# Performance work log

Hardware: AMD Instinct MI355X
Metric: run time of the kernel (lower is better)

The kernel has to match this reference:

```python
import jax, jax.numpy as jnp
import numpy as np
import math

E = 512
H = 2048
P = 128  # attention_limit

def _make_params(key):
    ks = jax.random.split(key, 6)
    s = 0.02
    p = {}
    p['wq'] = jax.random.normal(ks[0], (E, E), jnp.float32) * s
    p['bq'] = jnp.zeros((E,), jnp.float32)
    p['wk'] = jax.random.normal(ks[1], (E, E), jnp.float32) * s
    p['bk'] = jnp.zeros((E,), jnp.float32)
    p['wv'] = jax.random.normal(ks[2], (E, E), jnp.float32) * s
    p['bv'] = jnp.zeros((E,), jnp.float32)
    p['w1'] = jax.random.normal(ks[3], (E, H), jnp.float32) * s
    p['b1'] = jnp.zeros((H,), jnp.float32)
    p['w2'] = jax.random.normal(ks[4], (H, E), jnp.float32) * s
    p['b2'] = jnp.zeros((E,), jnp.float32)
    p['ln1_w'] = jnp.ones((E,), jnp.float32)
    p['ln1_b'] = jnp.zeros((E,), jnp.float32)
    p['ln2_w'] = jnp.ones((E,), jnp.float32)
    p['ln2_b'] = jnp.zeros((E,), jnp.float32)
    return p

def setup_inputs() -> dict:
    key = jax.random.key(0)
    kx, kp = jax.random.split(key)
    inp = {'x': jax.random.normal(kx, (2, 1024, E), jnp.float32)}
    inp.update(_make_params(kp))
    return inp

def _layernorm(x, w, b, eps=1e-5):
    mu = jnp.mean(x, axis=-1, keepdims=True)
    var = jnp.mean((x - mu) ** 2, axis=-1, keepdims=True)
    return (x - mu) / jnp.sqrt(var + eps) * w + b

def _forward(x, wq, bq, wk, bk, wv, bv, w1, b1, w2, b2, ln1_w, ln1_b, ln2_w, ln2_b):
    B, S, Ed = x.shape
    # "RoPE" is actually additive sinusoidal PE in the source
    pos = jnp.arange(S, dtype=jnp.float32)[:, None]
    div = jnp.exp(jnp.arange(0, Ed, 2, dtype=jnp.float32) * (-math.log(10000.0) / Ed))
    pe = jnp.zeros((S, Ed), jnp.float32)
    pe = pe.at[:, 0::2].set(jnp.sin(pos * div))
    pe = pe.at[:, 1::2].set(jnp.cos(pos * div))
    x = x + pe[None]

    # local attention: pad x first, then apply K/V linears (padded rows -> bias)
    x_ext = jnp.pad(x, ((0, 0), (P, P), (0, 0)))
    q = x @ wq + bq                      # [B,S,E]
    k_ext = x_ext @ wk + bk              # [B,S+2P,E]
    v_ext = x_ext @ wv + bv
    W = 2 * P + 1
    win_idx = jnp.arange(S)[:, None] + jnp.arange(W)[None, :]  # [S,W]
    k_win = k_ext[:, win_idx]            # [B,S,W,E]
    v_win = v_ext[:, win_idx]            # [B,S,W,E]
    energy = jnp.einsum('bse,bswe->bsw', q, k_win) / jnp.sqrt(jnp.float32(Ed))
    attn = jax.nn.softmax(energy, axis=-1)
    attn_out = jnp.einsum('bsw,bswe->bse', attn, v_win)

    x = _layernorm(attn_out + x, ln1_w, ln1_b)
    ff = jnp.maximum(x @ w1 + b1, 0.0) @ w2 + b2
    return _layernorm(ff + x, ln2_w, ln2_b)

def reference(x, wq, bq, wk, bk, wv, bv, w1, b1, w2, b2, ln1_w, ln1_b, ln2_w, ln2_b):
    return _forward(x, wq, bq, wk, bk, wv, bv, w1, b1, w2, b2, ln1_w, ln1_b, ln2_w, ln2_b)
```

## Files before the change

### kernel.cpp

```cpp
#include <hip/hip_runtime.h>
#include <hip/hip_bf16.h>

#define S_LEN 1024
#define E_DIM 512
#define H_DIM 2048
#define P_PAD 128
#define EXTA 1296
#define BS_ROWS 2048

typedef __attribute__((ext_vector_type(8))) short bf16x8;
typedef __attribute__((ext_vector_type(4))) float f32x4;

__device__ inline ushort f2bf(float x) {
  union { float f; unsigned u; } c; c.f = x;
  unsigned u = c.u;
  u += 0x7fffu + ((u >> 16) & 1u);
  return (ushort)(u >> 16);
}

__device__ inline void gload16(ushort* dst, const ushort* src) {
  __builtin_amdgcn_global_load_lds(
      (const __attribute__((address_space(1))) void*)src,
      (__attribute__((address_space(3))) void*)dst, 16, 0, 0);
}

__global__ __launch_bounds__(256) void transpose_all_kernel(const float* __restrict__ wq,
                                                            const float* __restrict__ wk,
                                                            const float* __restrict__ wv,
                                                            const float* __restrict__ w1,
                                                            const float* __restrict__ w2,
                                                            ushort* __restrict__ wqkvT,
                                                            ushort* __restrict__ w1T,
                                                            ushort* __restrict__ w2T) {
  __shared__ float t[32][33];
  const int tile = blockIdx.x;
  const float* W; ushort* WT; int K, N, bx, by;
  if (tile < 768) {
    K = 512; N = 512;
    int sect = tile >> 8, tt = tile & 255;
    W = sect == 0 ? wq : (sect == 1 ? wk : wv);
    WT = wqkvT + (size_t)sect * 512 * 512;
    bx = tt & 15; by = tt >> 4;
  } else if (tile < 1792) {
    K = 512; N = 2048; W = w1; WT = w1T;
    int tt = tile - 768; bx = tt & 63; by = tt >> 6;
  } else {
    K = 2048; N = 512; W = w2; WT = w2T;
    int tt = tile - 1792; bx = tt & 15; by = tt >> 4;
  }
  int lx = threadIdx.x & 31, ly = threadIdx.x >> 5;
  int n0 = bx * 32, k0 = by * 32;
#pragma unroll
  for (int r = 0; r < 4; ++r)
    t[ly + r * 8][lx] = W[(size_t)(k0 + ly + r * 8) * N + n0 + lx];
  __syncthreads();
#pragma unroll
  for (int r = 0; r < 4; ++r)
    WT[(size_t)(n0 + ly + r * 8) * K + k0 + lx] = f2bf(t[lx][ly + r * 8]);
}

__global__ __launch_bounds__(256) void pe_pad_kernel(const float* __restrict__ x,
                                                     const float* __restrict__ bk,
                                                     const float* __restrict__ bv,
                                                     float* __restrict__ xpe,
                                                     ushort* __restrict__ xpe_bf,
                                                     ushort* __restrict__ k_bf,
                                                     ushort* __restrict__ v_t) {
  int idx = blockIdx.x * 256 + threadIdx.x;
  if (idx < BS_ROWS * E_DIM) {
    int e = idx & (E_DIM - 1);
    int s = (idx >> 9) & (S_LEN - 1);
    const float c = -9.210340371976184f / 512.0f;
    float freq = expf((float)(e & ~1) * c);
    float ang = (float)s * freq;
    float pe = (e & 1) ? cosf(ang) : sinf(ang);
    float v = x[idx] + pe;
    xpe[idx] = v;
    xpe_bf[idx] = f2bf(v);
  } else {
    int p = idx - BS_ROWS * E_DIM;
    int t = p / (2 * 272 * 512);
    int r2 = p % (2 * 272 * 512);
    int b = r2 / (272 * 512);
    int r3 = r2 % (272 * 512);
    if (t == 0) {
      int rr = r3 >> 9, e = r3 & 511;
      int row = rr < 128 ? rr : 1024 + rr;
      float v = rr < 256 ? bk[e] : 0.f;
      k_bf[((size_t)b * EXTA + row) * 512 + e] = f2bf(v);
    } else {
      int n = r3 / 272, jj = r3 % 272;
      int j = jj < 128 ? jj : 1024 + jj;
      float v = jj < 256 ? bv[n] : 0.f;
      v_t[((size_t)b * 512 + n) * EXTA + j] = f2bf(v);
    }
  }
}

template <int BM, int BN, int WM, int WN, int OUT>
__global__ __launch_bounds__(256) void mfma_gemm(const ushort* __restrict__ A,
                                                 const ushort* __restrict__ Bt,
                                                 const float* __restrict__ bias,
                                                 const float* __restrict__ bias2,
                                                 const float* __restrict__ bias3,
                                                 void* __restrict__ Cout,
                                                 ushort* __restrict__ q_out,
                                                 ushort* __restrict__ k_out,
                                                 ushort* __restrict__ v_out,
                                                 int M, int N, int K, int LDA) {
  constexpr int WAVES_N = BN / WN;
  constexpr int FM = WM / 16, FN = WN / 16;
  __shared__ ushort As[BM * 64];
  __shared__ ushort Bs[BN * 64];
  const int tid = threadIdx.x;
  const int lane = tid & 63;
  const int w = tid >> 6;
  const int wr = w / WAVES_N, wc = w % WAVES_N;
  const int l15 = lane & 15, lhi = lane >> 4;
  const int col0 = blockIdx.x * BN, row0 = blockIdx.y * BM;
  const int koff = blockIdx.z * K;

  f32x4 acc[FM][FN] = {};

  for (int k0 = 0; k0 < K; k0 += 64) {
#pragma unroll
    for (int it = 0; it < BM / 32; ++it) {
      int u = it * 256 + tid;
      int r = u >> 3;
      int c16 = (u & 7) ^ (r & 7);
      gload16(&As[(size_t)u * 8], &A[(size_t)(row0 + r) * LDA + koff + k0 + c16 * 8]);
    }
#pragma unroll
    for (int it = 0; it < BN / 32; ++it) {
      int u = it * 256 + tid;
      int r = u >> 3;
      int c16 = (u & 7) ^ (r & 7);
      gload16(&Bs[(size_t)u * 8], &Bt[(size_t)(col0 + r) * LDA + koff + k0 + c16 * 8]);
    }
    __syncthreads();
#pragma unroll
    for (int kk = 0; kk < 2; ++kk) {
      bf16x8 af[FM], bfr[FN];
#pragma unroll
      for (int mi = 0; mi < FM; ++mi) {
        int r = wr * WM + mi * 16 + l15;
        int c16 = (kk * 4 + lhi) ^ (r & 7);
        af[mi] = *(const bf16x8*)&As[r * 64 + c16 * 8];
      }
#pragma unroll
      for (int ni = 0; ni < FN; ++ni) {
        int r = wc * WN + ni * 16 + l15;
        int c16 = (kk * 4 + lhi) ^ (r & 7);
        bfr[ni] = *(const bf16x8*)&Bs[r * 64 + c16 * 8];
      }
#pragma unroll
      for (int mi = 0; mi < FM; ++mi)
#pragma unroll
        for (int ni = 0; ni < FN; ++ni)
          acc[mi][ni] = __builtin_amdgcn_mfma_f32_16x16x32_bf16(af[mi], bfr[ni], acc[mi][ni], 0, 0, 0);
    }
    __syncthreads();
  }

#pragma unroll
  for (int mi = 0; mi < FM; ++mi) {
    int mbase = row0 + wr * WM + mi * 16 + lhi * 4;
#pragma unroll
    for (int ni = 0; ni < FN; ++ni) {
      int n = col0 + wc * WN + ni * 16 + l15;
      if constexpr (OUT == 0) {
        float b = bias[n];
        float* C = (float*)Cout;
#pragma unroll
        for (int j = 0; j < 4; ++j) C[(size_t)(mbase + j) * N + n] = acc[mi][ni][j] + b;
      } else if constexpr (OUT == 1) {
        float b = bias[n];
        ushort* C = (ushort*)Cout;
#pragma unroll
        for (int j = 0; j < 4; ++j) C[(size_t)(mbase + j) * N + n] = f2bf(fmaxf(acc[mi][ni][j] + b, 0.f));
      } else if constexpr (OUT == 3) {
        float* C = (float*)Cout + (size_t)blockIdx.z * M * N;
#pragma unroll
        for (int j = 0; j < 4; ++j) C[(size_t)(mbase + j) * N + n] = acc[mi][ni][j];
      } else {
        int sect = n >> 9, nn = n & 511;
        float b = sect == 0 ? bias[nn] : (sect == 1 ? bias2[nn] : bias3[nn]);
        int bb = mbase >> 10;
        int s = mbase & 1023;
        if (sect == 0) {
#pragma unroll
          for (int j = 0; j < 4; ++j) q_out[(size_t)(mbase + j) * 512 + nn] = f2bf(acc[mi][ni][j] + b);
        } else if (sect == 1) {
#pragma unroll
          for (int j = 0; j < 4; ++j)
            k_out[((size_t)bb * EXTA + 128 + s + j) * 512 + nn] = f2bf(acc[mi][ni][j] + b);
        } else {
          ushort4 pk;
          pk.x = f2bf(acc[mi][ni][0] + b);
          pk.y = f2bf(acc[mi][ni][1] + b);
          pk.z = f2bf(acc[mi][ni][2] + b);
          pk.w = f2bf(acc[mi][ni][3] + b);
          *(ushort4*)&v_out[((size_t)bb * 512 + nn) * EXTA + 128 + s] = pk;
        }
      }
    }
  }
}

__global__ __launch_bounds__(512) void attn_mfma(const ushort* __restrict__ qb,
                                                 const ushort* __restrict__ kb,
                                                 const ushort* __restrict__ vt,
                                                 float* __restrict__ out) {
  __shared__ float e_s[16][292];
  __shared__ ushort p_s[16][296];
  __shared__ float inv_s[16];
  const int tid = threadIdx.x;
  const int lane = tid & 63;
  const int w = tid >> 6;
  const int l15 = lane & 15, lhi = lane >> 4;
  const int tile = blockIdx.x;
  const int b = tile >> 6;
  const int s0 = (tile & 63) * 16;

  const ushort* qrow = qb + (size_t)(b * 1024 + s0 + l15) * 512 + lhi * 8;
  bf16x8 qf[16];
#pragma unroll
  for (int ks = 0; ks < 16; ++ks) qf[ks] = *(const bf16x8*)(qrow + ks * 32);

  const float scale = 0.044194173824159216f;
  const ushort* kbase = kb + (size_t)b * EXTA * 512 + (size_t)(s0 + l15) * 512 + lhi * 8;

  for (int jt = w; jt < 18; jt += 8) {
    f32x4 acc = {};
    const ushort* kp = kbase + (size_t)jt * 16 * 512;
#pragma unroll
    for (int ks = 0; ks < 16; ++ks) {
      bf16x8 kf = *(const bf16x8*)(kp + ks * 32);
      acc = __builtin_amdgcn_mfma_f32_16x16x32_bf16(qf[ks], kf, acc, 0, 0, 0);
    }
    int jc = jt * 16 + l15;
#pragma unroll
    for (int j = 0; j < 4; ++j) {
      int i = lhi * 4 + j;
      bool valid = (jc >= i) && (jc <= i + 256);
      e_s[i][jc] = valid ? acc[j] * scale : -1e30f;
    }
  }
  __syncthreads();

  {
    int r = tid >> 5, c0 = tid & 31;
    float m = -1e30f;
#pragma unroll
    for (int t = 0; t < 9; ++t) m = fmaxf(m, e_s[r][c0 + 32 * t]);
#pragma unroll
    for (int off = 1; off <= 16; off <<= 1) m = fmaxf(m, __shfl_xor(m, off));
    float s = 0.f;
#pragma unroll
    for (int t = 0; t < 9; ++t) {
      float p = __expf(e_s[r][c0 + 32 * t] - m);
      s += p;
      p_s[r][c0 + 32 * t] = f2bf(p);
    }
#pragma unroll
    for (int off = 1; off <= 16; off <<= 1) s += __shfl_xor(s, off);
    if (c0 == 0) inv_s[r] = 1.0f / s;
  }
  __syncthreads();

  bf16x8 pf[9];
#pragma unroll
  for (int ks = 0; ks < 9; ++ks) pf[ks] = *(const bf16x8*)&p_s[l15][ks * 32 + lhi * 8];
  float inv[4];
#pragma unroll
  for (int j = 0; j < 4; ++j) inv[j] = inv_s[lhi * 4 + j];

  const ushort* vbase = vt + (size_t)b * 512 * EXTA + s0 + lhi * 8;
  float* obase = out + (size_t)(b * 1024 + s0) * 512;
#pragma unroll
  for (int ni = 0; ni < 4; ++ni) {
    int n = w * 64 + ni * 16 + l15;
    f32x4 acc = {};
    const ushort* vp = vbase + (size_t)n * EXTA;
#pragma unroll
    for (int ks = 0; ks < 9; ++ks) {
      bf16x8 vf = *(const bf16x8*)(vp + ks * 32);
      acc = __builtin_amdgcn_mfma_f32_16x16x32_bf16(pf[ks], vf, acc, 0, 0, 0);
    }
#pragma unroll
    for (int j = 0; j < 4; ++j)
      obase[(size_t)(lhi * 4 + j) * 512 + n] = acc[j] * inv[j];
  }
}

__device__ inline float wave_reduce_sum(float v) {
#pragma unroll
  for (int off = 32; off >= 1; off >>= 1) v += __shfl_xor(v, off);
  return v;
}

__global__ __launch_bounds__(256) void ln_kernel(const float* __restrict__ a,
                                                 const float* __restrict__ a2,
                                                 const float* __restrict__ ab,
                                                 const float* __restrict__ rsd,
                                                 const float* __restrict__ w,
                                                 const float* __restrict__ bias,
                                                 float* __restrict__ out,
                                                 ushort* __restrict__ out_bf) {
  const int row = blockIdx.x;
  const int tid = threadIdx.x;
  __shared__ float red[8];
  const int e0 = tid * 2;
  const size_t base = (size_t)row * E_DIM + e0;
  float2 av = *(const float2*)(a + base);
  float2 rv = *(const float2*)(rsd + base);
  float x0 = av.x + rv.x, x1 = av.y + rv.y;
  if (a2) {
    float2 v2 = *(const float2*)(a2 + base);
    x0 += v2.x; x1 += v2.y;
  }
  if (ab) {
    float2 bb = *(const float2*)(ab + e0);
    x0 += bb.x; x1 += bb.y;
  }

  float sm = wave_reduce_sum(x0 + x1);
  if ((tid & 63) == 0) red[tid >> 6] = sm;
  __syncthreads();
  float mu = (red[0] + red[1] + red[2] + red[3]) * (1.0f / 512.0f);
  float d0 = x0 - mu, d1 = x1 - mu;
  float vs = wave_reduce_sum(d0 * d0 + d1 * d1);
  if ((tid & 63) == 0) red[4 + (tid >> 6)] = vs;
  __syncthreads();
  float var = (red[4] + red[5] + red[6] + red[7]) * (1.0f / 512.0f);
  float inv = rsqrtf(var + 1e-5f);
  float2 wv = *(const float2*)(w + e0);
  float2 bi = *(const float2*)(bias + e0);
  float o0 = d0 * inv * wv.x + bi.x;
  float o1 = d1 * inv * wv.y + bi.y;
  *(float2*)(out + base) = make_float2(o0, o1);
  if (out_bf) {
    ushort2 ob;
    ob.x = f2bf(o0);
    ob.y = f2bf(o1);
    *(ushort2*)(out_bf + base) = ob;
  }
}

extern "C" void kernel_launch(void* const* d_in, const int* in_sizes, int n_in,
                              void* d_out, int out_size, void* d_ws, size_t ws_size,
                              hipStream_t stream) {
  const float* x    = (const float*)d_in[0];
  const float* wq   = (const float*)d_in[1];
  const float* bq   = (const float*)d_in[2];
  const float* wk   = (const float*)d_in[3];
  const float* bk   = (const float*)d_in[4];
  const float* wv   = (const float*)d_in[5];
  const float* bv   = (const float*)d_in[6];
  const float* w1   = (const float*)d_in[7];
  const float* b1   = (const float*)d_in[8];
  const float* w2   = (const float*)d_in[9];
  const float* b2   = (const float*)d_in[10];
  const float* ln1w = (const float*)d_in[11];
  const float* ln1b = (const float*)d_in[12];
  const float* ln2w = (const float*)d_in[13];
  const float* ln2b = (const float*)d_in[14];

  char* W = (char*)d_ws;
  float*  x_pe   = (float*)(W);
  float*  attn_o = (float*)(W + (4u  << 20));
  ushort* xpebf  = (ushort*)(W + (8u  << 20));
  ushort* wqkvT  = (ushort*)(W + (10u << 20));
  ushort* w1T    = (ushort*)(W + (12u << 20));
  ushort* w2T    = (ushort*)(W + (14u << 20));
  ushort* q_bf   = (ushort*)(W + (16u << 20));
  ushort* k_bf   = (ushort*)(W + (18u << 20));
  ushort* v_t    = (ushort*)(W + (21u << 20));
  float*  x1     = (float*)(W + (24u << 20));
  ushort* x1bf   = (ushort*)(W + (28u << 20));
  ushort* ff1_bf = (ushort*)(W + (30u << 20));
  float*  ff2    = (float*)(W + (38u << 20));

  transpose_all_kernel<<<2816, 256, 0, stream>>>(wq, wk, wv, w1, w2, wqkvT, w1T, w2T);
  pe_pad_kernel<<<6272, 256, 0, stream>>>(x, bk, bv, x_pe, xpebf, k_bf, v_t);

  mfma_gemm<64, 128, 32, 64, 2><<<dim3(12, 32), 256, 0, stream>>>(
      xpebf, wqkvT, bq, bk, bv, nullptr, q_bf, k_bf, v_t, BS_ROWS, 1536, 512, 512);

  attn_mfma<<<128, 512, 0, stream>>>(q_bf, k_bf, v_t, attn_o);
  ln_kernel<<<BS_ROWS, 256, 0, stream>>>(attn_o, nullptr, nullptr, x_pe, ln1w, ln1b, x1, x1bf);

  mfma_gemm<64, 128, 32, 64, 1><<<dim3(16, 32), 256, 0, stream>>>(
      x1bf, w1T, b1, nullptr, nullptr, ff1_bf, nullptr, nullptr, nullptr, BS_ROWS, H_DIM, 512, 512);

  mfma_gemm<64, 64, 32, 32, 3><<<dim3(8, 32, 2), 256, 0, stream>>>(
      ff1_bf, w2T, nullptr, nullptr, nullptr, ff2, nullptr, nullptr, nullptr, BS_ROWS, E_DIM, 1024, 2048);

  ln_kernel<<<BS_ROWS, 256, 0, stream>>>(ff2, ff2 + (size_t)BS_ROWS * E_DIM, b2, x1,
                                         ln2w, ln2b, (float*)d_out, nullptr);
}
```

Measured before the change: 83.82 us.

## Fuse LayerNorm1 into attention epilogue and merge prep kernels

Merges the weight-transpose and PE/pad kernels into one launch, and folds the residual add plus LayerNorm1 into the attention kernel's epilogue, computing row statistics with shuffles and shared-memory reductions. This removes two launches and the fp32 round trip of the attention output through global memory. In exchange, the fused LN computes variance as E[x^2]-mu^2, which is slightly less numerically stable, and the attention kernel gains extra registers and a barrier.

```diff
diff --git a/kernel.cpp b/kernel.cpp
--- a/kernel.cpp
+++ b/kernel.cpp
@@ -24,50 +24,25 @@
       (__attribute__((address_space(3))) void*)dst, 16, 0, 0);
 }
 
-__global__ __launch_bounds__(256) void transpose_all_kernel(const float* __restrict__ wq,
-                                                            const float* __restrict__ wk,
-                                                            const float* __restrict__ wv,
-                                                            const float* __restrict__ w1,
-                                                            const float* __restrict__ w2,
-                                                            ushort* __restrict__ wqkvT,
-                                                            ushort* __restrict__ w1T,
-                                                            ushort* __restrict__ w2T) {
+__global__ __launch_bounds__(256) void prep_kernel(const float* __restrict__ x,
+                                                   const float* __restrict__ bk,
+                                                   const float* __restrict__ bv,
+                                                   const float* __restrict__ wq,
+                                                   const float* __restrict__ wk,
+                                                   const float* __restrict__ wv,
+                                                   const float* __restrict__ w1,
+                                                   const float* __restrict__ w2,
+                                                   float* __restrict__ xpe,
+                                                   ushort* __restrict__ xpe_bf,
+                                                   ushort* __restrict__ k_bf,
+                                                   ushort* __restrict__ v_t,
+                                                   ushort* __restrict__ wqkvT,
+                                                   ushort* __restrict__ w1T,
+                                                   ushort* __restrict__ w2T) {
   __shared__ float t[32][33];
-  const int tile = blockIdx.x;
-  const float* W; ushort* WT; int K, N, bx, by;
-  if (tile < 768) {
-    K = 512; N = 512;
-    int sect = tile >> 8, tt = tile & 255;
-    W = sect == 0 ? wq : (sect == 1 ? wk : wv);
-    WT = wqkvT + (size_t)sect * 512 * 512;
-    bx = tt & 15; by = tt >> 4;
-  } else if (tile < 1792) {
-    K = 512; N = 2048; W = w1; WT = w1T;
-    int tt = tile - 768; bx = tt & 63; by = tt >> 6;
-  } else {
-    K = 2048; N = 512; W = w2; WT = w2T;
-    int tt = tile - 1792; bx = tt & 15; by = tt >> 4;
-  }
-  int lx = threadIdx.x & 31, ly = threadIdx.x >> 5;
-  int n0 = bx * 32, k0 = by * 32;
-#pragma unroll
-  for (int r = 0; r < 4; ++r)
-    t[ly + r * 8][lx] = W[(size_t)(k0 + ly + r * 8) * N + n0 + lx];
-  __syncthreads();
-#pragma unroll
-  for (int r = 0; r < 4; ++r)
-    WT[(size_t)(n0 + ly + r * 8) * K + k0 + lx] = f2bf(t[lx][ly + r * 8]);
-}
-
-__global__ __launch_bounds__(256) void pe_pad_kernel(const float* __restrict__ x,
-                                                     const float* __restrict__ bk,
-                                                     const float* __restrict__ bv,
-                                                     float* __restrict__ xpe,
-                                                     ushort* __restrict__ xpe_bf,
-                                                     ushort* __restrict__ k_bf,
-                                                     ushort* __restrict__ v_t) {
-  int idx = blockIdx.x * 256 + threadIdx.x;
-  if (idx < BS_ROWS * E_DIM) {
+  const int blk = blockIdx.x;
+  if (blk < 4096) {
+    int idx = blk * 256 + threadIdx.x;
     int e = idx & (E_DIM - 1);
     int s = (idx >> 9) & (S_LEN - 1);
     const float c = -9.210340371976184f / 512.0f;
@@ -77,13 +52,13 @@
     float v = x[idx] + pe;
     xpe[idx] = v;
     xpe_bf[idx] = f2bf(v);
-  } else {
-    int p = idx - BS_ROWS * E_DIM;
-    int t = p / (2 * 272 * 512);
+  } else if (blk < 6272) {
+    int p = (blk - 4096) * 256 + threadIdx.x;
+    int t2 = p / (2 * 272 * 512);
     int r2 = p % (2 * 272 * 512);
     int b = r2 / (272 * 512);
     int r3 = r2 % (272 * 512);
-    if (t == 0) {
+    if (t2 == 0) {
       int rr = r3 >> 9, e = r3 & 511;
       int row = rr < 128 ? rr : 1024 + rr;
       float v = rr < 256 ? bk[e] : 0.f;
@@ -94,6 +69,31 @@
       float v = jj < 256 ? bv[n] : 0.f;
       v_t[((size_t)b * 512 + n) * EXTA + j] = f2bf(v);
     }
+  } else {
+    const int tile = blk - 6272;
+    const float* W; ushort* WT; int K, N, bx, by;
+    if (tile < 768) {
+      K = 512; N = 512;
+      int sect = tile >> 8, tt = tile & 255;
+      W = sect == 0 ? wq : (sect == 1 ? wk : wv);
+      WT = wqkvT + (size_t)sect * 512 * 512;
+      bx = tt & 15; by = tt >> 4;
+    } else if (tile < 1792) {
+      K = 512; N = 2048; W = w1; WT = w1T;
+      int tt = tile - 768; bx = tt & 63; by = tt >> 6;
+    } else {
+      K = 2048; N = 512; W = w2; WT = w2T;
+      int tt = tile - 1792; bx = tt & 15; by = tt >> 4;
+    }
+    int lx = threadIdx.x & 31, ly = threadIdx.x >> 5;
+    int n0 = bx * 32, k0 = by * 32;
+#pragma unroll
+    for (int r = 0; r < 4; ++r)
+      t[ly + r * 8][lx] = W[(size_t)(k0 + ly + r * 8) * N + n0 + lx];
+    __syncthreads();
+#pragma unroll
+    for (int r = 0; r < 4; ++r)
+      WT[(size_t)(n0 + ly + r * 8) * K + k0 + lx] = f2bf(t[lx][ly + r * 8]);
   }
 }
 
@@ -168,12 +168,7 @@
 #pragma unroll
     for (int ni = 0; ni < FN; ++ni) {
       int n = col0 + wc * WN + ni * 16 + l15;
-      if constexpr (OUT == 0) {
-        float b = bias[n];
-        float* C = (float*)Cout;
-#pragma unroll
-        for (int j = 0; j < 4; ++j) C[(size_t)(mbase + j) * N + n] = acc[mi][ni][j] + b;
-      } else if constexpr (OUT == 1) {
+      if constexpr (OUT == 1) {
         float b = bias[n];
         ushort* C = (ushort*)Cout;
 #pragma unroll
@@ -207,13 +202,20 @@
   }
 }
 
-__global__ __launch_bounds__(512) void attn_mfma(const ushort* __restrict__ qb,
-                                                 const ushort* __restrict__ kb,
-                                                 const ushort* __restrict__ vt,
-                                                 float* __restrict__ out) {
+__global__ __launch_bounds__(512) void attn_ln1(const ushort* __restrict__ qb,
+                                                const ushort* __restrict__ kb,
+                                                const ushort* __restrict__ vt,
+                                                const float* __restrict__ x_pe,
+                                                const float* __restrict__ ln1w,
+                                                const float* __restrict__ ln1b,
+                                                float* __restrict__ x1,
+                                                ushort* __restrict__ x1bf) {
   __shared__ float e_s[16][292];
   __shared__ ushort p_s[16][296];
   __shared__ float inv_s[16];
+  __shared__ float redS[8][16];
+  __shared__ float redQ[8][16];
+  __shared__ float mu_s[16], rs_s[16];
   const int tid = threadIdx.x;
   const int lane = tid & 63;
   const int w = tid >> 6;
@@ -221,8 +223,9 @@
   const int tile = blockIdx.x;
   const int b = tile >> 6;
   const int s0 = (tile & 63) * 16;
-
-  const ushort* qrow = qb + (size_t)(b * 1024 + s0 + l15) * 512 + lhi * 8;
+  const int base0 = b * 1024 + s0;
+
+  const ushort* qrow = qb + (size_t)(base0 + l15) * 512 + lhi * 8;
   bf16x8 qf[16];
 #pragma unroll
   for (int ks = 0; ks < 16; ++ks) qf[ks] = *(const bf16x8*)(qrow + ks * 32);
@@ -276,7 +279,7 @@
   for (int j = 0; j < 4; ++j) inv[j] = inv_s[lhi * 4 + j];
 
   const ushort* vbase = vt + (size_t)b * 512 * EXTA + s0 + lhi * 8;
-  float* obase = out + (size_t)(b * 1024 + s0) * 512;
+  float val[4][4];
 #pragma unroll
   for (int ni = 0; ni < 4; ++ni) {
     int n = w * 64 + ni * 16 + l15;
@@ -288,8 +291,54 @@
       acc = __builtin_amdgcn_mfma_f32_16x16x32_bf16(pf[ks], vf, acc, 0, 0, 0);
     }
 #pragma unroll
-    for (int j = 0; j < 4; ++j)
-      obase[(size_t)(lhi * 4 + j) * 512 + n] = acc[j] * inv[j];
+    for (int j = 0; j < 4; ++j) {
+      int r = lhi * 4 + j;
+      val[ni][j] = acc[j] * inv[j] + x_pe[(size_t)(base0 + r) * 512 + n];
+    }
+  }
+
+  float S[4], Q[4];
+#pragma unroll
+  for (int j = 0; j < 4; ++j) {
+    S[j] = 0.f; Q[j] = 0.f;
+#pragma unroll
+    for (int ni = 0; ni < 4; ++ni) { S[j] += val[ni][j]; Q[j] += val[ni][j] * val[ni][j]; }
+  }
+#pragma unroll
+  for (int off = 1; off <= 8; off <<= 1) {
+#pragma unroll
+    for (int j = 0; j < 4; ++j) {
+      S[j] += __shfl_xor(S[j], off);
+      Q[j] += __shfl_xor(Q[j], off);
+    }
+  }
+  if (l15 == 0) {
+#pragma unroll
+    for (int j = 0; j < 4; ++j) { redS[w][lhi * 4 + j] = S[j]; redQ[w][lhi * 4 + j] = Q[j]; }
+  }
+  __syncthreads();
+  if (tid < 16) {
+    float sS = 0.f, sQ = 0.f;
+#pragma unroll
+    for (int ww = 0; ww < 8; ++ww) { sS += redS[ww][tid]; sQ += redQ[ww][tid]; }
+    float mu = sS * (1.0f / 512.0f);
+    float var = sQ * (1.0f / 512.0f) - mu * mu;
+    mu_s[tid] = mu;
+    rs_s[tid] = rsqrtf(var + 1e-5f);
+  }
+  __syncthreads();
+
+#pragma unroll
+  for (int ni = 0; ni < 4; ++ni) {
+    int n = w * 64 + ni * 16 + l15;
+    float lw = ln1w[n], lb = ln1b[n];
+#pragma unroll
+    for (int j = 0; j < 4; ++j) {
+      int r = lhi * 4 + j;
+      float o = (val[ni][j] - mu_s[r]) * rs_s[r] * lw + lb;
+      x1[(size_t)(base0 + r) * 512 + n] = o;
+      x1bf[(size_t)(base0 + r) * 512 + n] = f2bf(o);
+    }
   }
 }
 
@@ -305,8 +354,7 @@
                                                  const float* __restrict__ rsd,
                                                  const float* __restrict__ w,
                                                  const float* __restrict__ bias,
-                                                 float* __restrict__ out,
-                                                 ushort* __restrict__ out_bf) {
+                                                 float* __restrict__ out) {
   const int row = blockIdx.x;
   const int tid = threadIdx.x;
   __shared__ float red[8];
@@ -315,11 +363,11 @@
   float2 av = *(const float2*)(a + base);
   float2 rv = *(const float2*)(rsd + base);
   float x0 = av.x + rv.x, x1 = av.y + rv.y;
-  if (a2) {
+  {
     float2 v2 = *(const float2*)(a2 + base);
     x0 += v2.x; x1 += v2.y;
   }
-  if (ab) {
+  {
     float2 bb = *(const float2*)(ab + e0);
     x0 += bb.x; x1 += bb.y;
   }
@@ -339,12 +387,6 @@
   float o0 = d0 * inv * wv.x + bi.x;
   float o1 = d1 * inv * wv.y + bi.y;
   *(float2*)(out + base) = make_float2(o0, o1);
-  if (out_bf) {
-    ushort2 ob;
-    ob.x = f2bf(o0);
-    ob.y = f2bf(o1);
-    *(ushort2*)(out_bf + base) = ob;
-  }
 }
 
 extern "C" void kernel_launch(void* const* d_in, const int* in_sizes, int n_in,
@@ -368,27 +410,25 @@
 
   char* W = (char*)d_ws;
   float*  x_pe   = (float*)(W);
-  float*  attn_o = (float*)(W + (4u  << 20));
-  ushort* xpebf  = (ushort*)(W + (8u  << 20));
-  ushort* wqkvT  = (ushort*)(W + (10u << 20));
-  ushort* w1T    = (ushort*)(W + (12u << 20));
-  ushort* w2T    = (ushort*)(W + (14u << 20));
-  ushort* q_bf   = (ushort*)(W + (16u << 20));
-  ushort* k_bf   = (ushort*)(W + (18u << 20));
-  ushort* v_t    = (ushort*)(W + (21u << 20));
-  float*  x1     = (float*)(W + (24u << 20));
-  ushort* x1bf   = (ushort*)(W + (28u << 20));
-  ushort* ff1_bf = (ushort*)(W + (30u << 20));
-  float*  ff2    = (float*)(W + (38u << 20));
-
-  transpose_all_kernel<<<2816, 256, 0, stream>>>(wq, wk, wv, w1, w2, wqkvT, w1T, w2T);
-  pe_pad_kernel<<<6272, 256, 0, stream>>>(x, bk, bv, x_pe, xpebf, k_bf, v_t);
+  ushort* xpebf  = (ushort*)(W + (4u  << 20));
+  ushort* wqkvT  = (ushort*)(W + (6u  << 20));
+  ushort* w1T    = (ushort*)(W + (8u  << 20));
+  ushort* w2T    = (ushort*)(W + (10u << 20));
+  ushort* q_bf   = (ushort*)(W + (12u << 20));
+  ushort* k_bf   = (ushort*)(W + (14u << 20));
+  ushort* v_t    = (ushort*)(W + (17u << 20));
+  float*  x1     = (float*)(W + (20u << 20));
+  ushort* x1bf   = (ushort*)(W + (24u << 20));
+  ushort* ff1_bf = (ushort*)(W + (26u << 20));
+  float*  ff2    = (float*)(W + (34u << 20));
+
+  prep_kernel<<<9088, 256, 0, stream>>>(x, bk, bv, wq, wk, wv, w1, w2,
+                                        x_pe, xpebf, k_bf, v_t, wqkvT, w1T, w2T);
 
   mfma_gemm<64, 128, 32, 64, 2><<<dim3(12, 32), 256, 0, stream>>>(
       xpebf, wqkvT, bq, bk, bv, nullptr, q_bf, k_bf, v_t, BS_ROWS, 1536, 512, 512);
 
-  attn_mfma<<<128, 512, 0, stream>>>(q_bf, k_bf, v_t, attn_o);
-  ln_kernel<<<BS_ROWS, 256, 0, stream>>>(attn_o, nullptr, nullptr, x_pe, ln1w, ln1b, x1, x1bf);
+  attn_ln1<<<128, 512, 0, stream>>>(q_bf, k_bf, v_t, x_pe, ln1w, ln1b, x1, x1bf);
 
   mfma_gemm<64, 128, 32, 64, 1><<<dim3(16, 32), 256, 0, stream>>>(
       x1bf, w1T, b1, nullptr, nullptr, ff1_bf, nullptr, nullptr, nullptr, BS_ROWS, H_DIM, 512, 512);
@@ -397,5 +437,5 @@
       ff1_bf, w2T, nullptr, nullptr, nullptr, ff2, nullptr, nullptr, nullptr, BS_ROWS, E_DIM, 1024, 2048);
 
   ln_kernel<<<BS_ROWS, 256, 0, stream>>>(ff2, ff2 + (size_t)BS_ROWS * E_DIM, b2, x1,
-                                         ln2w, ln2b, (float*)d_out, nullptr);
-}
+                                         ln2w, ln2b, (float*)d_out);
+}
```

After: 77.08 us. 1.09x faster.
